# Optimization experiments

Measured on AMD Instinct MI355X. Metric: run time of the kernel, lower is better.

The kernel has to match this reference:

```python
import jax, jax.numpy as jnp
import numpy as np

DIM = 384
HEADS = 12
POS_DIM = (DIM // 4) // 4  # DynamicPosBias: pos_dim = (dim//4)//4 = 24
B_WIN = 64
GH = GW = GD = 8
N_TOK = GH * GW * GD  # 512
NG = 8  # num windows sharing one mask


def _ln(x, g, b):
    m = jnp.mean(x, axis=-1, keepdims=True)
    v = jnp.var(x, axis=-1, keepdims=True)
    return (x - m) / jnp.sqrt(v + 1e-5) * g + b


def setup_inputs() -> dict:
    key = jax.random.key(0)
    ks = jax.random.split(key, 8)
    s = 0.02
    inp = {
        "x": jax.random.normal(ks[0], (B_WIN, N_TOK, DIM), jnp.float32),
        "H": GH, "W": GW, "D": GD,
        "mask": jnp.zeros((NG, N_TOK, N_TOK), jnp.float32),
        "qkv_w": jax.random.normal(ks[1], (DIM, 3 * DIM), jnp.float32) * s,
        "qkv_b": jnp.zeros((3 * DIM,), jnp.float32),
        "proj_w": jax.random.normal(ks[2], (DIM, DIM), jnp.float32) * s,
        "proj_b": jnp.zeros((DIM,), jnp.float32),
        "pos_proj_w": jax.random.normal(ks[3], (3, POS_DIM), jnp.float32) * s,
        "pos_proj_b": jnp.zeros((POS_DIM,), jnp.float32),
        "ln1_g": jnp.ones((POS_DIM,), jnp.float32), "ln1_b": jnp.zeros((POS_DIM,), jnp.float32),
        "pos1_w": jax.random.normal(ks[4], (POS_DIM, POS_DIM), jnp.float32) * s,
        "pos1_b": jnp.zeros((POS_DIM,), jnp.float32),
        "ln2_g": jnp.ones((POS_DIM,), jnp.float32), "ln2_b": jnp.zeros((POS_DIM,), jnp.float32),
        "pos2_w": jax.random.normal(ks[5], (POS_DIM, POS_DIM), jnp.float32) * s,
        "pos2_b": jnp.zeros((POS_DIM,), jnp.float32),
        "ln3_g": jnp.ones((POS_DIM,), jnp.float32), "ln3_b": jnp.zeros((POS_DIM,), jnp.float32),
        "pos3_w": jax.random.normal(ks[6], (POS_DIM, HEADS), jnp.float32) * s,
        "pos3_b": jnp.zeros((HEADS,), jnp.float32),
    }
    return inp


def reference(x, H, W, D, mask, qkv_w, qkv_b, proj_w, proj_b,
              pos_proj_w, pos_proj_b, ln1_g, ln1_b, pos1_w, pos1_b,
              ln2_g, ln2_b, pos2_w, pos2_b, ln3_g, ln3_b, pos3_w, pos3_b):
    B_, N, C = x.shape
    h = HEADS
    d = C // h
    scale = d ** (-0.5)

    qkv = (x @ qkv_w + qkv_b).reshape(B_, N, 3, h, d).transpose(2, 0, 3, 1, 4)
    q, k, v = qkv[0] * scale, qkv[1], qkv[2]  # each (B_, h, N, d)

    attn = jnp.einsum('bhnd,bhmd->bhnm', q, k)  # (B_, h, N, N)

    # dynamic relative position bias
    rh = jnp.arange(1 - H, H)
    rw = jnp.arange(1 - W, W)
    rd = jnp.arange(1 - D, D)
    biases = jnp.stack(jnp.meshgrid(rh, rw, rd, indexing='ij'))
    biases = biases.reshape(3, -1).T.astype(jnp.float32)  # (L, 3), L=(2H-1)(2W-1)(2D-1)

    coords = jnp.stack(jnp.meshgrid(jnp.arange(H), jnp.arange(W), jnp.arange(D), indexing='ij'))
    coords = coords.reshape(3, -1)  # (3, N)
    rel = (coords[:, :, None] - coords[:, None, :]).transpose(1, 2, 0)  # (N, N, 3)
    rel = rel + jnp.array([H - 1, W - 1, D - 1])
    rel = rel * jnp.array([(2 * W - 1) * (2 * D - 1), 2 * D - 1, 1])
    rpi = rel.sum(-1)  # (N, N) int index into L

    pos = biases @ pos_proj_w + pos_proj_b  # (L, pos_dim)
    pos = jax.nn.relu(_ln(pos, ln1_g, ln1_b)) @ pos1_w + pos1_b
    pos = jax.nn.relu(_ln(pos, ln2_g, ln2_b)) @ pos2_w + pos2_b
    pos = jax.nn.relu(_ln(pos, ln3_g, ln3_b)) @ pos3_w + pos3_b  # (L, h)

    rel_bias = pos[rpi]  # (N, N, h)
    attn = attn + rel_bias.transpose(2, 0, 1)[None]  # (B_, h, N, N)

    nG = mask.shape[0]
    attn = attn.reshape(B_ // nG, nG, h, N, N) + mask[None, :, None]
    attn = jax.nn.softmax(attn.reshape(B_, h, N, N), axis=-1)

    out = jnp.einsum('bhnm,bhmd->bhnd', attn, v)  # (B_, h, N, d)
    out = out.transpose(0, 2, 1, 3).reshape(B_, N, C)
    return out @ proj_w + proj_b
```

## Files before the change

### kernel.cpp

```cpp
#include <hip/hip_runtime.h>


typedef __bf16 bf16;
typedef __bf16 bf16x4 __attribute__((ext_vector_type(4)));
typedef __bf16 bf16x8 __attribute__((ext_vector_type(8)));
typedef float  f32x4  __attribute__((ext_vector_type(4)));
typedef unsigned int u32;
typedef u32 u32x4v __attribute__((ext_vector_type(4)));

#define DIMC   384
#define HEADS  12
#define HD     32
#define NTOK   512
#define NWIN   64
#define LTAB   3375
#define LPAD   3392
#define PD     24
#define LOG2E  1.4426950408889634f
#define QPRE   (0.17677669529663687f * LOG2E)
#define VSTR   520

#define SZ_WQT  884736ll
#define SZ_WPT  294912ll
#define SZ_POST 81408ll
#define SZ_FLAG 256ll
#define SZ_B2   6291456ll
#define SZ_MT   4194304ll
#define SZ_QKV  25165824ll
#define WS_SMALL 102236160ull
#define WS_BIG   112410368ull

__device__ inline u32 cvtpk(float lo, float hi) {
    u32 r;
    asm("v_cvt_pk_bf16_f32 %0, %1, %2" : "=v"(r) : "v"(lo), "v"(hi));
    return r;
}
__device__ inline void plswap32(u32& a, u32& b) {
    asm("v_permlane32_swap_b32 %0, %1" : "+v"(a), "+v"(b));
}
__device__ inline void plswap16(u32& a, u32& b) {
    asm("v_permlane16_swap_b32 %0, %1" : "+v"(a), "+v"(b));
}
__device__ inline float ex2(float x) {
#if __has_builtin(__builtin_amdgcn_exp2f)
    return __builtin_amdgcn_exp2f(x);
#else
    float r; asm("v_exp_f32 %0, %1" : "=v"(r) : "v"(x)); return r;
#endif
}
__device__ inline void gload_lds16(const void* g, void* l) {
    __builtin_amdgcn_global_load_lds(
        (const __attribute__((address_space(1))) void*)g,
        (__attribute__((address_space(3))) void*)l, 16, 0, 0);
}

__global__ __launch_bounds__(256) void transpose_kernel(
    const float* __restrict__ src, bf16* __restrict__ dst, int K, int N)
{
    int idx = blockIdx.x * 256 + threadIdx.x;
    if (idx >= K * N) return;
    int n = idx / K, k = idx - n * K;
    dst[idx] = (bf16)src[(size_t)k * N + n];
}

__global__ __launch_bounds__(256) void xcast_kernel(
    const float* __restrict__ src, bf16* __restrict__ dst)
{
    const int i = blockIdx.x * 256 + threadIdx.x;
    const f32x4 v = *(const f32x4*)(src + (size_t)i * 4);
    bf16x4 o;
#pragma unroll
    for (int j = 0; j < 4; j++) o[j] = (bf16)v[j];
    *(bf16x4*)(dst + (size_t)i * 4) = o;
}

__global__ __launch_bounds__(256) void mask_detect_kernel(
    const float* __restrict__ mask, int* __restrict__ flag)
{
    int i = blockIdx.x * 256 + threadIdx.x;
    const float* p = mask + (size_t)i * 32;
    float s = 0.f;
#pragma unroll
    for (int j = 0; j < 32; j++) s += fabsf(p[j]);
    if (!(s == 0.f)) atomicOr(flag, 1);
}

__device__ inline void ln_relu24(const float* x, const float* __restrict__ g,
                                 const float* __restrict__ b, float* y)
{
    float mean = 0.f;
#pragma unroll
    for (int j = 0; j < PD; j++) mean += x[j];
    mean *= (1.f / PD);
    float var = 0.f;
#pragma unroll
    for (int j = 0; j < PD; j++) { float d = x[j] - mean; var += d * d; }
    var *= (1.f / PD);
    float inv = rsqrtf(var + 1e-5f);
#pragma unroll
    for (int j = 0; j < PD; j++) {
        float t = (x[j] - mean) * inv * g[j] + b[j];
        y[j] = t > 0.f ? t : 0.f;
    }
}

__global__ __launch_bounds__(256) void pos_mlp_kernel(
    const float* __restrict__ pw,  const float* __restrict__ pb,
    const float* __restrict__ g1,  const float* __restrict__ b1,
    const float* __restrict__ w1,  const float* __restrict__ bb1,
    const float* __restrict__ g2,  const float* __restrict__ b2,
    const float* __restrict__ w2,  const float* __restrict__ bb2,
    const float* __restrict__ g3,  const float* __restrict__ b3,
    const float* __restrict__ w3,  const float* __restrict__ bb3,
    bf16* __restrict__ posTg)
{
    int l = blockIdx.x * 256 + threadIdx.x;
    if (l >= LTAB) return;
    int ih = l / 225, iw = (l / 15) % 15, id = l % 15;
    float c0 = (float)(ih - 7), c1 = (float)(iw - 7), c2 = (float)(id - 7);
    float x[PD], y[PD];
#pragma unroll
    for (int j = 0; j < PD; j++)
        x[j] = c0 * pw[j] + c1 * pw[PD + j] + c2 * pw[2 * PD + j] + pb[j];
    ln_relu24(x, g1, b1, y);
#pragma unroll
    for (int j = 0; j < PD; j++) {
        float a = bb1[j];
#pragma unroll
        for (int i = 0; i < PD; i++) a += y[i] * w1[i * PD + j];
        x[j] = a;
    }
    ln_relu24(x, g2, b2, y);
#pragma unroll
    for (int j = 0; j < PD; j++) {
        float a = bb2[j];
#pragma unroll
        for (int i = 0; i < PD; i++) a += y[i] * w2[i * PD + j];
        x[j] = a;
    }
    ln_relu24(x, g3, b3, y);
#pragma unroll
    for (int hh = 0; hh < HEADS; hh++) {
        float a = bb3[hh];
#pragma unroll
        for (int i = 0; i < PD; i++) a += y[i] * w3[i * HEADS + hh];
        posTg[hh * LPAD + l] = (bf16)(a * LOG2E);
    }
}

__global__ __launch_bounds__(256) void bias2_build_kernel(
    const bf16* __restrict__ posTg, bf16* __restrict__ bias2)
{
    int idx = blockIdx.x * 256 + threadIdx.x;
    int h = idx >> 18;
    int q = (idx >> 9) & 511;
    int m = idx & 511;
    int dh = (q >> 6) - (m >> 6) + 7;
    int dw = ((q >> 3) & 7) - ((m >> 3) & 7) + 7;
    int dd = (q & 7) - (m & 7) + 7;
    bias2[idx] = posTg[h * LPAD + dh * 225 + dw * 15 + dd];
}

template <int MODE>
__global__ __launch_bounds__(256) void gemm_bt(
    const bf16* __restrict__ A, const bf16* __restrict__ Bt,
    const float* __restrict__ bias,
    bf16* __restrict__ O0, bf16* __restrict__ O1, bf16* __restrict__ O2,
    float* __restrict__ Of, int K, int N)
{
    __shared__ __align__(16) bf16 lA[128 * 64];
    __shared__ __align__(16) bf16 lB[128 * 64];
    const int row0 = blockIdx.x * 128;
    const int col0 = blockIdx.y * 128;
    const int tid  = threadIdx.x;
    const int lane = tid & 63;
    const int wave = tid >> 6;
    const int r0   = (wave >> 1) * 64;
    const int c0   = (wave & 1) * 64;
    const int lrow = lane & 15;
    const int lch  = lane >> 4;

    f32x4 acc[4][4];
    const f32x4 zero4 = {0.f, 0.f, 0.f, 0.f};
#pragma unroll
    for (int i = 0; i < 4; i++)
#pragma unroll
        for (int j = 0; j < 4; j++) acc[i][j] = zero4;

    for (int kt = 0; kt < K; kt += 64) {
        __syncthreads();
#pragma unroll
        for (int it = 0; it < 4; it++) {
            const int c  = tid + it * 256;
            const int rr = c >> 3;
            const int cc = (c & 7) * 8;
            bf16* la = lA + (size_t)(it * 256 + wave * 64) * 8;
            bf16* lb = lB + (size_t)(it * 256 + wave * 64) * 8;
            gload_lds16(A  + (size_t)(row0 + rr) * K + kt + cc, la);
            gload_lds16(Bt + (size_t)(col0 + rr) * K + kt + cc, lb);
        }
        __syncthreads();
#pragma unroll
        for (int kk = 0; kk < 64; kk += 32) {
            bf16x8 af[4], bfr[4];
#pragma unroll
            for (int i = 0; i < 4; i++)
                af[i] = *(const bf16x8*)(lA + (r0 + i * 16 + lrow) * 64 + kk + lch * 8);
#pragma unroll
            for (int j = 0; j < 4; j++)
                bfr[j] = *(const bf16x8*)(lB + (c0 + j * 16 + lrow) * 64 + kk + lch * 8);
#pragma unroll
            for (int i = 0; i < 4; i++)
#pragma unroll
                for (int j = 0; j < 4; j++)
                    acc[i][j] = __builtin_amdgcn_mfma_f32_16x16x32_bf16(af[i], bfr[j], acc[i][j], 0, 0, 0);
        }
    }

#pragma unroll
    for (int i = 0; i < 4; i++) {
#pragma unroll
        for (int j = 0; j < 4; j++) {
#pragma unroll
            for (int r = 0; r < 4; r++) {
                const int mrow = row0 + r0 + i * 16 + lch * 4 + r;
                const int ncol = col0 + c0 + j * 16 + lrow;
                const float v = acc[i][j][r] + bias[ncol];
                if (MODE == 0) {
                    const int t    = ncol >= 768 ? 2 : (ncol >= 384 ? 1 : 0);
                    const int rem2 = ncol - t * 384;
                    const int hh   = rem2 >> 5;
                    const int dd   = rem2 & 31;
                    const int bwin = mrow >> 9;
                    const int n    = mrow & 511;
                    bf16* dst = (t == 0) ? O0 : ((t == 1) ? O1 : O2);
                    const float vv = (t == 0) ? v * QPRE : v;
                    dst[(size_t)((bwin * HEADS + hh) * NTOK + n) * HD + dd] = (bf16)vv;
                } else {
                    Of[(size_t)mrow * N + ncol] = v;
                }
            }
        }
    }
}

template <int BIG>
__global__ __launch_bounds__(256, 4) void attn_kernel(
    const bf16* __restrict__ Qg, const bf16* __restrict__ Kg,
    const bf16* __restrict__ Vg, const bf16* __restrict__ posTg,
    const float* __restrict__ maskg, const bf16* __restrict__ bias2,
    const int* __restrict__ mflag, bf16* __restrict__ Og)
{
    __shared__ __align__(16) bf16 lVt[32 * VSTR];
    __shared__ __align__(16) bf16 lPos[BIG ? 16 : LPAD];

    const int idx = blockIdx.x;
    const int h   = idx >> 8;
    const int rem = idx & 255;
    const int b   = rem >> 2;
    const int qt  = rem & 3;
    const int g   = b & 7;
    const int tid = threadIdx.x;
    const int lane = tid & 63;
    const int wave = tid >> 6;
    const int lrow = lane & 15;
    const int lch  = lane >> 4;
    const int msk  = *mflag;

    const bf16* Qp  = Qg + (size_t)(b * HEADS + h) * NTOK * HD;
    const bf16* Kp  = Kg + (size_t)(b * HEADS + h) * NTOK * HD;
    const bf16* Vp  = Vg + (size_t)(b * HEADS + h) * NTOK * HD;
    const float* Mp = maskg + (size_t)g * NTOK * NTOK;
    const bf16* B2p = bias2 + (size_t)h * NTOK * NTOK;

    for (int n = tid; n < NTOK; n += 256) {
        const bf16* vsrc = Vp + n * HD;
        bf16x8 v0 = *(const bf16x8*)(vsrc);
        bf16x8 v1 = *(const bf16x8*)(vsrc + 8);
        bf16x8 v2 = *(const bf16x8*)(vsrc + 16);
        bf16x8 v3 = *(const bf16x8*)(vsrc + 24);
#pragma unroll
        for (int c = 0; c < 8; c++) {
            lVt[(c)      * VSTR + n] = v0[c];
            lVt[(8 + c)  * VSTR + n] = v1[c];
            lVt[(16 + c) * VSTR + n] = v2[c];
            lVt[(24 + c) * VSTR + n] = v3[c];
        }
    }
    if (!BIG) {
        const uint4* src = (const uint4*)(posTg + h * LPAD);
        for (int i = tid; i < LPAD * 2 / 16; i += 256)
            ((uint4*)lPos)[i] = src[i];
    }
    __syncthreads();

    const int qbase = qt * 128 + wave * 32;

    bf16x8 qf[2];
#pragma unroll
    for (int t = 0; t < 2; t++)
        qf[t] = *(const bf16x8*)(Qp + (size_t)(qbase + t * 16 + lrow) * HD + lch * 8);

    int qc0[2] = {0, 0}, qc1[2] = {0, 0}, qc2[2] = {0, 0};
    if (!BIG) {
#pragma unroll
        for (int t = 0; t < 2; t++) {
            const int q = qbase + t * 16 + lrow;
            qc0[t] = q >> 6; qc1[t] = (q >> 3) & 7; qc2[t] = q & 7;
        }
    }

    float m_i[2] = {-1e30f, -1e30f};
    float l_i[2] = {0.f, 0.f};
    f32x4 oacc[2][2];
    const f32x4 zero4 = {0.f, 0.f, 0.f, 0.f};
    oacc[0][0] = zero4; oacc[0][1] = zero4;
    oacc[1][0] = zero4; oacc[1][1] = zero4;

    for (int kt = 0; kt < 4; kt++) {
        bf16x8 apc[2][4];
        float alr[2];

#pragma unroll
        for (int t = 0; t < 2; t++) {
            const int qrow = qbase + t * 16 + lrow;
            f32x4 sf[8];

            bf16x4 bld[8];
            if (BIG) {
                const bf16* brow = B2p + (size_t)qrow * NTOK + kt * 128 + lch * 4;
#pragma unroll
                for (int ct = 0; ct < 8; ct++)
                    bld[ct] = *(const bf16x4*)(brow + ct * 16);
            }

#pragma unroll
            for (int ct = 0; ct < 8; ct++) {
                bf16x8 kf = *(const bf16x8*)(Kp + (size_t)(kt * 128 + ct * 16 + lrow) * HD + lch * 8);
                sf[ct] = __builtin_amdgcn_mfma_f32_16x16x32_bf16(kf, qf[t], zero4, 0, 0, 0);
            }

            if (BIG) {
#pragma unroll
                for (int ct = 0; ct < 8; ct++)
#pragma unroll
                    for (int r = 0; r < 4; r++)
                        sf[ct][r] += (float)bld[ct][r];
            } else {
#pragma unroll
                for (int ct = 0; ct < 8; ct++) {
#pragma unroll
                    for (int r = 0; r < 4; r++) {
                        const int k = kt * 128 + ct * 16 + lch * 4 + r;
                        const int rpi = (qc0[t] - (k >> 6) + 7) * 225
                                      + (qc1[t] - ((k >> 3) & 7) + 7) * 15
                                      + (qc2[t] - (k & 7) + 7);
                        sf[ct][r] += (float)lPos[rpi];
                    }
                }
            }
            if (msk) {
                const float* mrow = Mp + (size_t)qrow * NTOK + kt * 128 + lch * 4;
#pragma unroll
                for (int ct = 0; ct < 8; ct++) {
                    f32x4 mv = *(const f32x4*)(mrow + ct * 16);
#pragma unroll
                    for (int r = 0; r < 4; r++)
                        sf[ct][r] = fmaf(mv[r], LOG2E, sf[ct][r]);
                }
            }

            float px[8];
#pragma unroll
            for (int ct = 0; ct < 8; ct++)
                px[ct] = fmaxf(fmaxf(sf[ct][0], sf[ct][1]), fmaxf(sf[ct][2], sf[ct][3]));
            float mx = fmaxf(fmaxf(fmaxf(px[0], px[1]), fmaxf(px[2], px[3])),
                             fmaxf(fmaxf(px[4], px[5]), fmaxf(px[6], px[7])));
            mx = fmaxf(mx, __shfl_xor(mx, 16));
            mx = fmaxf(mx, __shfl_xor(mx, 32));
            const float mnew = fmaxf(m_i[t], mx);
            const float al   = ex2(m_i[t] - mnew);
            m_i[t] = mnew;
            alr[t] = al;

            float s0 = 0.f, s1 = 0.f;
#pragma unroll
            for (int ct = 0; ct < 8; ct++) {
#pragma unroll
                for (int r = 0; r < 4; r++)
                    sf[ct][r] = ex2(sf[ct][r] - mnew);
                s0 += sf[ct][0] + sf[ct][1];
                s1 += sf[ct][2] + sf[ct][3];
            }
            float ls = s0 + s1;
            ls += __shfl_xor(ls, 16);
            ls += __shfl_xor(ls, 32);
            l_i[t] = l_i[t] * al + ls;

#pragma unroll
            for (int c2 = 0; c2 < 4; c2++) {
                u32 a01 = cvtpk(sf[2 * c2][0],     sf[2 * c2][1]);
                u32 a23 = cvtpk(sf[2 * c2][2],     sf[2 * c2][3]);
                u32 b01 = cvtpk(sf[2 * c2 + 1][0], sf[2 * c2 + 1][1]);
                u32 b23 = cvtpk(sf[2 * c2 + 1][2], sf[2 * c2 + 1][3]);
                plswap32(a01, b01); plswap16(a01, b01);
                plswap32(a23, b23); plswap16(a23, b23);
                u32x4v w; w[0] = a01; w[1] = a23; w[2] = b01; w[3] = b23;
                apc[t][c2] = __builtin_bit_cast(bf16x8, w);
            }
        }

#pragma unroll
        for (int t = 0; t < 2; t++) {
#pragma unroll
            for (int r = 0; r < 4; r++) {
                const float a = __shfl(alr[t], lch * 4 + r);
                oacc[t][0][r] *= a;
                oacc[t][1][r] *= a;
            }
        }

#pragma unroll
        for (int c2 = 0; c2 < 4; c2++) {
            const int mofs = kt * 128 + c2 * 32;
            bf16x8 bv0 = *(const bf16x8*)(lVt + (size_t)lrow * VSTR + mofs + lch * 8);
            bf16x8 bv1 = *(const bf16x8*)(lVt + (size_t)(16 + lrow) * VSTR + mofs + lch * 8);
#pragma unroll
            for (int t = 0; t < 2; t++) {
                oacc[t][0] = __builtin_amdgcn_mfma_f32_16x16x32_bf16(apc[t][c2], bv0, oacc[t][0], 0, 0, 0);
                oacc[t][1] = __builtin_amdgcn_mfma_f32_16x16x32_bf16(apc[t][c2], bv1, oacc[t][1], 0, 0, 0);
            }
        }
    }

#pragma unroll
    for (int t = 0; t < 2; t++) {
#pragma unroll
        for (int r = 0; r < 4; r++) {
            const float lv  = __shfl(l_i[t], lch * 4 + r);
            const float inv = 1.f / fmaxf(lv, 1e-20f);
            const int n = qbase + t * 16 + lch * 4 + r;
            bf16* orow = Og + (size_t)(b * NTOK + n) * DIMC + h * HD;
            orow[lrow]      = (bf16)(oacc[t][0][r] * inv);
            orow[16 + lrow] = (bf16)(oacc[t][1][r] * inv);
        }
    }
}

extern "C" void kernel_launch(void* const* d_in, const int* in_sizes, int n_in,
                              void* d_out, int out_size, void* d_ws, size_t ws_size,
                              hipStream_t stream)
{
    if (ws_size < WS_SMALL) return;
    const bool BIG = (ws_size >= WS_BIG);

    const float* x      = (const float*)d_in[0];
    const float* maskp  = (const float*)d_in[4];
    const float* qkv_w  = (const float*)d_in[5];
    const float* qkv_b  = (const float*)d_in[6];
    const float* proj_w = (const float*)d_in[7];
    const float* proj_b = (const float*)d_in[8];

    char* ws = (char*)d_ws;
    size_t off = 0;
    bf16* wsWqT  = (bf16*)(ws + off); off += SZ_WQT;
    bf16* wsWpT  = (bf16*)(ws + off); off += SZ_WPT;
    bf16* wsPosT = (bf16*)(ws + off); off += SZ_POST;
    int*  wsFlag = (int*)(ws + off);  off += SZ_FLAG;
    bf16* wsB2 = nullptr;
    if (BIG) {
        wsB2 = (bf16*)(ws + off); off += SZ_B2;
        off += SZ_MT;
    } else {
        off = 1572864;
    }
    bf16* wsQ    = (bf16*)(ws + off); off += SZ_QKV;
    bf16* wsK    = (bf16*)(ws + off); off += SZ_QKV;
    bf16* wsV    = (bf16*)(ws + off); off += SZ_QKV;
    bf16* wsAttn = (bf16*)(ws + off);
    bf16* wsXb   = wsAttn;

    hipMemsetAsync(wsFlag, 0, 4, stream);
    mask_detect_kernel<<<256, 256, 0, stream>>>(maskp, wsFlag);

    transpose_kernel<<<(384 * 1152 + 255) / 256, 256, 0, stream>>>(qkv_w, wsWqT, 384, 1152);
    transpose_kernel<<<(384 * 384 + 255) / 256, 256, 0, stream>>>(proj_w, wsWpT, 384, 384);
    pos_mlp_kernel<<<(LTAB + 255) / 256, 256, 0, stream>>>(
        (const float*)d_in[9],  (const float*)d_in[10], (const float*)d_in[11],
        (const float*)d_in[12], (const float*)d_in[13], (const float*)d_in[14],
        (const float*)d_in[15], (const float*)d_in[16], (const float*)d_in[17],
        (const float*)d_in[18], (const float*)d_in[19], (const float*)d_in[20],
        (const float*)d_in[21], (const float*)d_in[22], wsPosT);

    xcast_kernel<<<(32768 * 384 / 4) / 256, 256, 0, stream>>>(x, wsXb);

    if (BIG)
        bias2_build_kernel<<<(HEADS * NTOK * NTOK) / 256, 256, 0, stream>>>(wsPosT, wsB2);

    gemm_bt<0><<<dim3(256, 9), 256, 0, stream>>>(wsXb, wsWqT, qkv_b, wsQ, wsK, wsV,
                                                 nullptr, 384, 1152);

    if (BIG)
        attn_kernel<1><<<HEADS * NWIN * 4, 256, 0, stream>>>(
            wsQ, wsK, wsV, wsPosT, maskp, wsB2, wsFlag, wsAttn);
    else
        attn_kernel<0><<<HEADS * NWIN * 4, 256, 0, stream>>>(
            wsQ, wsK, wsV, wsPosT, maskp, wsB2, wsFlag, wsAttn);

    gemm_bt<1><<<dim3(256, 3), 256, 0, stream>>>(wsAttn, wsWpT, proj_b,
                                                 nullptr, nullptr, nullptr,
                                                 (float*)d_out, 384, 384);
}
```

Measured before the change: 422.0 us.

## Fuse prep kernels and pre-transpose V globally to drop LDS staging in attention

Merges the x cast, the two weight transposes, the mask detection and the position MLP into a single prep kernel that dispatches work by block index, cutting launch overhead. A separate kernel transposes V in place per window-head, so the attention kernel reads V^T fragments straight from global memory. The per-block LDS V transpose, its barrier and the 32x520 LDS buffer go away, and the occupancy hint rises from 4 to 8 blocks. The costs are an extra pass over V and global (cache-dependent) reads for the V operand inside the attention inner loop, since the four query-tile blocks of each window-head now each read V from global memory.

```diff
diff --git a/kernel.cpp b/kernel.cpp
--- a/kernel.cpp
+++ b/kernel.cpp
@@ -18,7 +18,6 @@
 #define PD     24
 #define LOG2E  1.4426950408889634f
 #define QPRE   (0.17677669529663687f * LOG2E)
-#define VSTR   520
 
 #define SZ_WQT  884736ll
 #define SZ_WPT  294912ll
@@ -30,6 +29,13 @@
 #define WS_SMALL 102236160ull
 #define WS_BIG   112410368ull
 
+#define NB_XC   12288
+#define NB_WQT  1728
+#define NB_WPT  576
+#define NB_MSK  256
+#define NB_POS  14
+#define NB_PREP (NB_XC + NB_WQT + NB_WPT + NB_MSK + NB_POS)
+
 __device__ inline u32 cvtpk(float lo, float hi) {
     u32 r;
     asm("v_cvt_pk_bf16_f32 %0, %1, %2" : "=v"(r) : "v"(lo), "v"(hi));
@@ -54,37 +60,6 @@
         (__attribute__((address_space(3))) void*)l, 16, 0, 0);
 }
 
-__global__ __launch_bounds__(256) void transpose_kernel(
-    const float* __restrict__ src, bf16* __restrict__ dst, int K, int N)
-{
-    int idx = blockIdx.x * 256 + threadIdx.x;
-    if (idx >= K * N) return;
-    int n = idx / K, k = idx - n * K;
-    dst[idx] = (bf16)src[(size_t)k * N + n];
-}
-
-__global__ __launch_bounds__(256) void xcast_kernel(
-    const float* __restrict__ src, bf16* __restrict__ dst)
-{
-    const int i = blockIdx.x * 256 + threadIdx.x;
-    const f32x4 v = *(const f32x4*)(src + (size_t)i * 4);
-    bf16x4 o;
-#pragma unroll
-    for (int j = 0; j < 4; j++) o[j] = (bf16)v[j];
-    *(bf16x4*)(dst + (size_t)i * 4) = o;
-}
-
-__global__ __launch_bounds__(256) void mask_detect_kernel(
-    const float* __restrict__ mask, int* __restrict__ flag)
-{
-    int i = blockIdx.x * 256 + threadIdx.x;
-    const float* p = mask + (size_t)i * 32;
-    float s = 0.f;
-#pragma unroll
-    for (int j = 0; j < 32; j++) s += fabsf(p[j]);
-    if (!(s == 0.f)) atomicOr(flag, 1);
-}
-
 __device__ inline void ln_relu24(const float* x, const float* __restrict__ g,
                                  const float* __restrict__ b, float* y)
 {
@@ -104,7 +79,10 @@
     }
 }
 
-__global__ __launch_bounds__(256) void pos_mlp_kernel(
+__global__ __launch_bounds__(256) void prep_kernel(
+    const float* __restrict__ x,
+    const float* __restrict__ qkv_w, const float* __restrict__ proj_w,
+    const float* __restrict__ mask,
     const float* __restrict__ pw,  const float* __restrict__ pb,
     const float* __restrict__ g1,  const float* __restrict__ b1,
     const float* __restrict__ w1,  const float* __restrict__ bb1,
@@ -112,39 +90,79 @@
     const float* __restrict__ w2,  const float* __restrict__ bb2,
     const float* __restrict__ g3,  const float* __restrict__ b3,
     const float* __restrict__ w3,  const float* __restrict__ bb3,
-    bf16* __restrict__ posTg)
-{
-    int l = blockIdx.x * 256 + threadIdx.x;
-    if (l >= LTAB) return;
-    int ih = l / 225, iw = (l / 15) % 15, id = l % 15;
-    float c0 = (float)(ih - 7), c1 = (float)(iw - 7), c2 = (float)(id - 7);
-    float x[PD], y[PD];
-#pragma unroll
-    for (int j = 0; j < PD; j++)
-        x[j] = c0 * pw[j] + c1 * pw[PD + j] + c2 * pw[2 * PD + j] + pb[j];
-    ln_relu24(x, g1, b1, y);
-#pragma unroll
-    for (int j = 0; j < PD; j++) {
-        float a = bb1[j];
-#pragma unroll
-        for (int i = 0; i < PD; i++) a += y[i] * w1[i * PD + j];
-        x[j] = a;
-    }
-    ln_relu24(x, g2, b2, y);
-#pragma unroll
-    for (int j = 0; j < PD; j++) {
-        float a = bb2[j];
-#pragma unroll
-        for (int i = 0; i < PD; i++) a += y[i] * w2[i * PD + j];
-        x[j] = a;
-    }
-    ln_relu24(x, g3, b3, y);
-#pragma unroll
-    for (int hh = 0; hh < HEADS; hh++) {
-        float a = bb3[hh];
-#pragma unroll
-        for (int i = 0; i < PD; i++) a += y[i] * w3[i * HEADS + hh];
-        posTg[hh * LPAD + l] = (bf16)(a * LOG2E);
+    bf16* __restrict__ xb, bf16* __restrict__ wqT, bf16* __restrict__ wpT,
+    int* __restrict__ flag, bf16* __restrict__ posTg)
+{
+    const int tid = threadIdx.x;
+    int bx = blockIdx.x;
+
+    if (bx < NB_XC) {
+        const int i = bx * 256 + tid;
+        const f32x4 v = *(const f32x4*)(x + (size_t)i * 4);
+        bf16x4 o;
+#pragma unroll
+        for (int j = 0; j < 4; j++) o[j] = (bf16)v[j];
+        *(bf16x4*)(xb + (size_t)i * 4) = o;
+        return;
+    }
+    bx -= NB_XC;
+    if (bx < NB_WQT) {
+        const int idx = bx * 256 + tid;
+        const int n = idx / 384, k = idx - n * 384;
+        wqT[idx] = (bf16)qkv_w[(size_t)k * 1152 + n];
+        return;
+    }
+    bx -= NB_WQT;
+    if (bx < NB_WPT) {
+        const int idx = bx * 256 + tid;
+        const int n = idx / 384, k = idx - n * 384;
+        wpT[idx] = (bf16)proj_w[(size_t)k * 384 + n];
+        return;
+    }
+    bx -= NB_WPT;
+    if (bx < NB_MSK) {
+        const int i = bx * 256 + tid;
+        const float* p = mask + (size_t)i * 32;
+        float s = 0.f;
+#pragma unroll
+        for (int j = 0; j < 32; j++) s += fabsf(p[j]);
+        if (!(s == 0.f)) atomicOr(flag, 1);
+        return;
+    }
+    bx -= NB_MSK;
+    {
+        const int l = bx * 256 + tid;
+        if (l >= LTAB) return;
+        const int ih = l / 225, iw = (l / 15) % 15, id = l % 15;
+        const float c0 = (float)(ih - 7), c1 = (float)(iw - 7), c2 = (float)(id - 7);
+        float xx[PD], y[PD];
+#pragma unroll
+        for (int j = 0; j < PD; j++)
+            xx[j] = c0 * pw[j] + c1 * pw[PD + j] + c2 * pw[2 * PD + j] + pb[j];
+        ln_relu24(xx, g1, b1, y);
+#pragma unroll
+        for (int j = 0; j < PD; j++) {
+            float a = bb1[j];
+#pragma unroll
+            for (int i = 0; i < PD; i++) a += y[i] * w1[i * PD + j];
+            xx[j] = a;
+        }
+        ln_relu24(xx, g2, b2, y);
+#pragma unroll
+        for (int j = 0; j < PD; j++) {
+            float a = bb2[j];
+#pragma unroll
+            for (int i = 0; i < PD; i++) a += y[i] * w2[i * PD + j];
+            xx[j] = a;
+        }
+        ln_relu24(xx, g3, b3, y);
+#pragma unroll
+        for (int hh = 0; hh < HEADS; hh++) {
+            float a = bb3[hh];
+#pragma unroll
+            for (int i = 0; i < PD; i++) a += y[i] * w3[i * HEADS + hh];
+            posTg[hh * LPAD + l] = (bf16)(a * LOG2E);
+        }
     }
 }
 
@@ -159,6 +177,34 @@
     int dw = ((q >> 3) & 7) - ((m >> 3) & 7) + 7;
     int dd = (q & 7) - (m & 7) + 7;
     bias2[idx] = posTg[h * LPAD + dh * 225 + dw * 15 + dd];
+}
+
+__global__ __launch_bounds__(256) void vt_inplace_kernel(bf16* __restrict__ V)
+{
+    __shared__ __align__(16) bf16 tile[32 * 520];
+    bf16* base = V + (size_t)blockIdx.x * (NTOK * HD);
+    const int tid = threadIdx.x;
+    const int nq = tid >> 2;
+    const int c4 = tid & 3;
+    const int d0 = c4 * 8;
+#pragma unroll
+    for (int it = 0; it < 8; it++) {
+        const int n = nq + it * 64;
+        bf16x8 v = *(const bf16x8*)(base + n * HD + d0);
+#pragma unroll
+        for (int j = 0; j < 8; j++) {
+            const int jj = (j + (c4 << 1)) & 7;
+            tile[(d0 + jj) * 520 + n] = v[jj];
+        }
+    }
+    __syncthreads();
+#pragma unroll
+    for (int it = 0; it < 8; it++) {
+        const int o = it * 2048 + tid * 8;
+        const int d = o >> 9, n = o & 511;
+        bf16x8 w = *(const bf16x8*)(tile + d * 520 + n);
+        *(bf16x8*)(base + d * NTOK + n) = w;
+    }
 }
 
 template <int MODE>
@@ -245,13 +291,12 @@
 }
 
 template <int BIG>
-__global__ __launch_bounds__(256, 4) void attn_kernel(
+__global__ __launch_bounds__(256, 8) void attn_kernel(
     const bf16* __restrict__ Qg, const bf16* __restrict__ Kg,
-    const bf16* __restrict__ Vg, const bf16* __restrict__ posTg,
+    const bf16* __restrict__ Vtg, const bf16* __restrict__ posTg,
     const float* __restrict__ maskg, const bf16* __restrict__ bias2,
     const int* __restrict__ mflag, bf16* __restrict__ Og)
 {
-    __shared__ __align__(16) bf16 lVt[32 * VSTR];
     __shared__ __align__(16) bf16 lPos[BIG ? 16 : LPAD];
 
     const int idx = blockIdx.x;
@@ -267,32 +312,18 @@
     const int lch  = lane >> 4;
     const int msk  = *mflag;
 
-    const bf16* Qp  = Qg + (size_t)(b * HEADS + h) * NTOK * HD;
-    const bf16* Kp  = Kg + (size_t)(b * HEADS + h) * NTOK * HD;
-    const bf16* Vp  = Vg + (size_t)(b * HEADS + h) * NTOK * HD;
+    const bf16* Qp  = Qg  + (size_t)(b * HEADS + h) * NTOK * HD;
+    const bf16* Kp  = Kg  + (size_t)(b * HEADS + h) * NTOK * HD;
+    const bf16* Vtp = Vtg + (size_t)(b * HEADS + h) * NTOK * HD;
     const float* Mp = maskg + (size_t)g * NTOK * NTOK;
     const bf16* B2p = bias2 + (size_t)h * NTOK * NTOK;
 
-    for (int n = tid; n < NTOK; n += 256) {
-        const bf16* vsrc = Vp + n * HD;
-        bf16x8 v0 = *(const bf16x8*)(vsrc);
-        bf16x8 v1 = *(const bf16x8*)(vsrc + 8);
-        bf16x8 v2 = *(const bf16x8*)(vsrc + 16);
-        bf16x8 v3 = *(const bf16x8*)(vsrc + 24);
-#pragma unroll
-        for (int c = 0; c < 8; c++) {
-            lVt[(c)      * VSTR + n] = v0[c];
-            lVt[(8 + c)  * VSTR + n] = v1[c];
-            lVt[(16 + c) * VSTR + n] = v2[c];
-            lVt[(24 + c) * VSTR + n] = v3[c];
-        }
-    }
     if (!BIG) {
         const uint4* src = (const uint4*)(posTg + h * LPAD);
         for (int i = tid; i < LPAD * 2 / 16; i += 256)
             ((uint4*)lPos)[i] = src[i];
-    }
-    __syncthreads();
+        __syncthreads();
+    }
 
     const int qbase = qt * 128 + wave * 32;
 
@@ -423,8 +454,8 @@
 #pragma unroll
         for (int c2 = 0; c2 < 4; c2++) {
             const int mofs = kt * 128 + c2 * 32;
-            bf16x8 bv0 = *(const bf16x8*)(lVt + (size_t)lrow * VSTR + mofs + lch * 8);
-            bf16x8 bv1 = *(const bf16x8*)(lVt + (size_t)(16 + lrow) * VSTR + mofs + lch * 8);
+            bf16x8 bv0 = *(const bf16x8*)(Vtp + (size_t)lrow * NTOK + mofs + lch * 8);
+            bf16x8 bv1 = *(const bf16x8*)(Vtp + (size_t)(16 + lrow) * NTOK + mofs + lch * 8);
 #pragma unroll
             for (int t = 0; t < 2; t++) {
                 oacc[t][0] = __builtin_amdgcn_mfma_f32_16x16x32_bf16(apc[t][c2], bv0, oacc[t][0], 0, 0, 0);
@@ -481,24 +512,23 @@
     bf16* wsXb   = wsAttn;
 
     hipMemsetAsync(wsFlag, 0, 4, stream);
-    mask_detect_kernel<<<256, 256, 0, stream>>>(maskp, wsFlag);
-
-    transpose_kernel<<<(384 * 1152 + 255) / 256, 256, 0, stream>>>(qkv_w, wsWqT, 384, 1152);
-    transpose_kernel<<<(384 * 384 + 255) / 256, 256, 0, stream>>>(proj_w, wsWpT, 384, 384);
-    pos_mlp_kernel<<<(LTAB + 255) / 256, 256, 0, stream>>>(
+
+    prep_kernel<<<NB_PREP, 256, 0, stream>>>(
+        x, qkv_w, proj_w, maskp,
         (const float*)d_in[9],  (const float*)d_in[10], (const float*)d_in[11],
         (const float*)d_in[12], (const float*)d_in[13], (const float*)d_in[14],
         (const float*)d_in[15], (const float*)d_in[16], (const float*)d_in[17],
         (const float*)d_in[18], (const float*)d_in[19], (const float*)d_in[20],
-        (const float*)d_in[21], (const float*)d_in[22], wsPosT);
-
-    xcast_kernel<<<(32768 * 384 / 4) / 256, 256, 0, stream>>>(x, wsXb);
+        (const float*)d_in[21], (const float*)d_in[22],
+        wsXb, wsWqT, wsWpT, wsFlag, wsPosT);
 
     if (BIG)
         bias2_build_kernel<<<(HEADS * NTOK * NTOK) / 256, 256, 0, stream>>>(wsPosT, wsB2);
 
     gemm_bt<0><<<dim3(256, 9), 256, 0, stream>>>(wsXb, wsWqT, qkv_b, wsQ, wsK, wsV,
                                                  nullptr, 384, 1152);
+
+    vt_inplace_kernel<<<NWIN * HEADS, 256, 0, stream>>>(wsV);
 
     if (BIG)
         attn_kernel<1><<<HEADS * NWIN * 4, 256, 0, stream>>>(
```

Measured after the change: 556.4 us. 31.9% more time.
